# Performance work log

Measured on AMD Instinct MI355X. Metric: run time of the kernel, lower is better.

The kernel has to match this reference:

```python
import jax, jax.numpy as jnp
import numpy as np

N_NODES = 50000
N_EDGES = 1600000
NEG_SLOPE = 0.2


def setup_inputs() -> dict:
    key = jax.random.key(0)
    ks = jax.random.split(key, 11)
    s = 0.1  # small init scale
    return {
        "x": jax.random.normal(ks[0], (N_NODES, 128), dtype=jnp.float32),
        "edge_index": jax.random.randint(ks[1], (2, N_EDGES), 0, N_NODES, dtype=jnp.int64),
        "W1": jax.random.normal(ks[2], (128, 128), dtype=jnp.float32) * s,
        "att_src1": jax.random.normal(ks[3], (2, 64), dtype=jnp.float32) * s,
        "att_dst1": jax.random.normal(ks[4], (2, 64), dtype=jnp.float32) * s,
        "b1": jax.random.normal(ks[5], (128,), dtype=jnp.float32) * s,
        "W2": jax.random.normal(ks[6], (128, 64), dtype=jnp.float32) * s,
        "att_src2": jax.random.normal(ks[7], (1, 64), dtype=jnp.float32) * s,
        "att_dst2": jax.random.normal(ks[8], (1, 64), dtype=jnp.float32) * s,
        "b2": jax.random.normal(ks[9], (64,), dtype=jnp.float32) * s,
    }


def gat_conv(x, W, a_src, a_dst, bias, src, dst, n_nodes):
    # x: [N, F_in]; W: [F_in, H*C]; a_src/a_dst: [H, C]; bias: [H*C]
    H, C = a_src.shape
    xl = (x @ W).reshape(n_nodes, H, C)                 # [N,H,C]
    alpha_s = jnp.einsum('nhc,hc->nh', xl, a_src)       # [N,H]
    alpha_d = jnp.einsum('nhc,hc->nh', xl, a_dst)       # [N,H]
    e = jax.nn.leaky_relu(alpha_s[src] + alpha_d[dst], NEG_SLOPE)  # [E,H]
    # segment softmax over edges sharing the same destination node
    m = jax.ops.segment_max(e, dst, num_segments=n_nodes)          # [N,H]
    m = jnp.where(jnp.isfinite(m), m, 0.0)
    e = jnp.exp(e - m[dst])
    denom = jax.ops.segment_sum(e, dst, num_segments=n_nodes)      # [N,H]
    alpha = e / denom[dst]                               # self-loops guarantee denom > 0
    msg = xl[src] * alpha[:, :, None]                    # [E,H,C]
    out = jax.ops.segment_sum(msg, dst, num_segments=n_nodes)      # [N,H,C]
    return out.reshape(n_nodes, H * C) + bias


def reference(x, edge_index, W1, att_src1, att_dst1, b1, W2, att_src2, att_dst2, b2):
    n = x.shape[0]
    # PyG GATConv default add_self_loops=True
    loops = jnp.arange(n, dtype=edge_index.dtype)
    src = jnp.concatenate([edge_index[0], loops])
    dst = jnp.concatenate([edge_index[1], loops])

    h = gat_conv(x, W1, att_src1, att_dst1, b1, src, dst, n)   # [N, 128]
    h = jax.nn.relu(h)                                          # dropout p=0 (eval)
    h = gat_conv(h, W2, att_src2, att_dst2, b2, src, dst, n)   # [N, 64]
    h = jax.nn.relu(h)
    return h
```

## Files before the change

kernel.cpp:

```cpp
#include <hip/hip_runtime.h>
#include <cstdint>
#include <cstddef>

#define NEG_SLOPE 0.2f

#define NB 512
#define LOG_NB 9
#define MAXK 512

__device__ inline unsigned short f2bf(float f) {
    unsigned int u = __float_as_uint(f);
    u += 0x7FFFu + ((u >> 16) & 1u);
    return (unsigned short)(u >> 16);
}
__device__ inline float bf_lo(unsigned int u) { return __uint_as_float(u << 16); }
__device__ inline float bf_hi(unsigned int u) { return __uint_as_float(u & 0xFFFF0000u); }

__global__ __launch_bounds__(256) void sort_count_kernel(const int* __restrict__ ei, int E,
                                                         int K, int CH, int* __restrict__ bcnt) {
    __shared__ int hist[MAXK];
    int tid = threadIdx.x;
    for (int i = tid; i < K; i += 256) hist[i] = 0;
    __syncthreads();
    int lo = blockIdx.x * CH;
    int hi = lo + CH; if (hi > E) hi = E;
    for (int e = lo + tid; e < hi; e += 256)
        atomicAdd(&hist[ei[(size_t)E + e] >> LOG_NB], 1);
    __syncthreads();
    for (int i = tid; i < K; i += 256)
        if (hist[i]) atomicAdd(&bcnt[i], hist[i]);
}

__global__ void sort_scan_kernel(const int* __restrict__ bcnt, int* __restrict__ boff,
                                 int* __restrict__ bcur, int K, int E) {
    __shared__ int buf[MAXK];
    int tid = threadIdx.x;
    int v = (tid < K) ? bcnt[tid] : 0;
    buf[tid] = v;
    __syncthreads();
    for (int o = 1; o < MAXK; o <<= 1) {
        int t = (tid >= o) ? buf[tid - o] : 0;
        __syncthreads();
        buf[tid] += t;
        __syncthreads();
    }
    if (tid < K) {
        int ex = buf[tid] - v;
        boff[tid] = ex;
        bcur[tid] = ex;
    }
    if (tid == K) boff[K] = E;
}

__global__ __launch_bounds__(256) void sort_scatter_kernel(const int* __restrict__ ei, int E,
                                                           int K, int CH, int* __restrict__ bcur,
                                                           unsigned int* __restrict__ bkt) {
    __shared__ int hist[MAXK];
    __shared__ int base[MAXK];
    int tid = threadIdx.x;
    for (int i = tid; i < K; i += 256) hist[i] = 0;
    __syncthreads();
    int lo = blockIdx.x * CH;
    int hi = lo + CH; if (hi > E) hi = E;
    for (int e = lo + tid; e < hi; e += 256)
        atomicAdd(&hist[ei[(size_t)E + e] >> LOG_NB], 1);
    __syncthreads();
    for (int i = tid; i < K; i += 256) {
        int c = hist[i];
        base[i] = c ? atomicAdd(&bcur[i], c) : 0;
    }
    __syncthreads();
    for (int i = tid; i < K; i += 256) hist[i] = 0;
    __syncthreads();
    for (int e = lo + tid; e < hi; e += 256) {
        int s = ei[e];
        int d = ei[(size_t)E + e];
        int k = d >> LOG_NB;
        int r = atomicAdd(&hist[k], 1);
        bkt[(size_t)base[k] + r] = (unsigned int)s | ((unsigned int)d << 16);
    }
}

__global__ __launch_bounds__(256) void sort_finalize_kernel(const unsigned int* __restrict__ bkt,
                                                            const int* __restrict__ boff,
                                                            int* __restrict__ off,
                                                            int* __restrict__ csrc, int N) {
    __shared__ int nhist[NB];
    __shared__ int part[256];
    __shared__ int loff[NB];
    int k = blockIdx.x;
    int tid = threadIdx.x;
    int node0 = k << LOG_NB;
    int nh = N - node0; if (nh > NB) nh = NB;
    int beg = boff[k], end = boff[k + 1];
    for (int i = tid; i < NB; i += 256) nhist[i] = 0;
    __syncthreads();
    for (int e = beg + tid; e < end; e += 256)
        atomicAdd(&nhist[(bkt[e] >> 16) - node0], 1);
    __syncthreads();
    int i0 = 2 * tid, i1 = 2 * tid + 1;
    int v0 = (i0 < nh) ? nhist[i0] + 1 : 0;
    int v1 = (i1 < nh) ? nhist[i1] + 1 : 0;
    part[tid] = v0 + v1;
    __syncthreads();
    for (int o = 1; o < 256; o <<= 1) {
        int t = (tid >= o) ? part[tid - o] : 0;
        __syncthreads();
        part[tid] += t;
        __syncthreads();
    }
    int gbase = beg + node0;
    int base = gbase + ((tid > 0) ? part[tid - 1] : 0);
    if (i0 < nh) loff[i0] = base;
    if (i1 < nh) loff[i1] = base + v0;
    __syncthreads();
    for (int i = tid; i < nh; i += 256) {
        off[node0 + i] = loff[i];
        csrc[loff[i]] = node0 + i;
        nhist[i] = loff[i] + 1;
    }
    if (node0 + nh == N && tid == 0) off[N] = gbase + part[255];
    __syncthreads();
    for (int e = beg + tid; e < end; e += 256) {
        unsigned int p = bkt[e];
        int pos = atomicAdd(&nhist[(p >> 16) - node0], 1);
        csrc[pos] = (int)(p & 0xFFFFu);
    }
}


template <int FOUT, int H>
__global__ __launch_bounds__(256) void gemm_att_kernel(const float* __restrict__ X,
                                                       const float* __restrict__ W,
                                                       const float* __restrict__ attS,
                                                       const float* __restrict__ attD,
                                                       unsigned short* __restrict__ Ybf,
                                                       float* __restrict__ as_,
                                                       float* __restrict__ ad_, int N) {
    constexpr int ROWS = 8192 / FOUT;
    constexpr int CG   = FOUT / 4;
    __shared__ float sX[ROWS][68];
    __shared__ float sW[64 * FOUT];
    int tid = threadIdx.x;
    int rowbase = blockIdx.x * ROWS;
    int cg = tid % CG;
    int rg = tid / CG;
    int r0 = rg * 8;

    float acc[8][4];
#pragma unroll
    for (int i = 0; i < 8; i++)
#pragma unroll
        for (int c = 0; c < 4; c++) acc[i][c] = 0.f;

    for (int k0 = 0; k0 < 128; k0 += 64) {
        __syncthreads();
        for (int idx = tid; idx < ROWS * 16; idx += 256) {
            int r = idx >> 4, q = idx & 15;
            int row = rowbase + r;
            float4 val = (row < N) ? *(const float4*)&X[(size_t)row * 128 + k0 + q * 4]
                                   : make_float4(0.f, 0.f, 0.f, 0.f);
            *(float4*)&sX[r][q * 4] = val;
        }
        for (int idx = tid; idx < 16 * FOUT; idx += 256)
            *(float4*)&sW[idx * 4] = *(const float4*)&W[(size_t)k0 * FOUT + idx * 4];
        __syncthreads();
        for (int k = 0; k < 64; k += 4) {
            float4 xr[8];
#pragma unroll
            for (int i = 0; i < 8; i++)
                xr[i] = *(const float4*)&sX[r0 + i][k];
#pragma unroll
            for (int kk = 0; kk < 4; kk++) {
                float4 wv = ((const float4*)(sW + (size_t)(k + kk) * FOUT))[cg];
#pragma unroll
                for (int i = 0; i < 8; i++) {
                    float xv = (&xr[i].x)[kk];
                    acc[i][0] = fmaf(xv, wv.x, acc[i][0]);
                    acc[i][1] = fmaf(xv, wv.y, acc[i][1]);
                    acc[i][2] = fmaf(xv, wv.z, acc[i][2]);
                    acc[i][3] = fmaf(xv, wv.w, acc[i][3]);
                }
            }
        }
    }

#pragma unroll
    for (int i = 0; i < 8; i++) {
        int row = rowbase + r0 + i;
        if (row < N) {
            ushort4 v;
            v.x = f2bf(acc[i][0]); v.y = f2bf(acc[i][1]);
            v.z = f2bf(acc[i][2]); v.w = f2bf(acc[i][3]);
            *(ushort4*)(Ybf + (size_t)row * FOUT + cg * 4) = v;
        }
    }

    float4 asv = ((const float4*)attS)[cg];
    float4 adv = ((const float4*)attD)[cg];
    int head = (H == 2) ? (cg >> 4) : 0;
#pragma unroll
    for (int i = 0; i < 8; i++) {
        float ps = acc[i][0] * asv.x + acc[i][1] * asv.y + acc[i][2] * asv.z + acc[i][3] * asv.w;
        float pd = acc[i][0] * adv.x + acc[i][1] * adv.y + acc[i][2] * adv.z + acc[i][3] * adv.w;
#pragma unroll
        for (int o = 1; o <= 8; o <<= 1) { ps += __shfl_xor(ps, o); pd += __shfl_xor(pd, o); }
        int row = rowbase + r0 + i;
        if ((tid & 15) == 0 && row < N) {
            as_[(size_t)row * H + head] = ps;
            ad_[(size_t)row * H + head] = pd;
        }
    }
}


__global__ __launch_bounds__(256) void agg1_kernel(const unsigned short* __restrict__ xl,
                                                   const float* __restrict__ as_,
                                                   const float* __restrict__ ad_,
                                                   const float* __restrict__ bias,
                                                   const int* __restrict__ off,
                                                   const int* __restrict__ csrc,
                                                   float* __restrict__ out, int N) {
    __shared__ float4 sps[4][64];
    int wiw  = threadIdx.x >> 6;
    int lane = threadIdx.x & 63;
    int node = blockIdx.x * 4 + wiw;
    if (node >= N) return;
    int beg = off[node], end = off[node + 1];
    int deg = end - beg;
    float2 adn = ((const float2*)ad_)[node];

    int cl  = lane & 15;
    int sub = lane >> 4;
    int hd1 = (cl >> 3) & 1;
    float acc[8];
#pragma unroll
    for (int i = 0; i < 8; i++) acc[i] = 0.f;
    const uint4* xq = (const uint4*)xl + cl;

    if (deg <= 64) {
        int s = 0;
        float t0 = -1e30f, t1 = -1e30f;
        if (lane < deg) {
            s = csrc[beg + lane];
            float2 asv = ((const float2*)as_)[s];
            t0 = asv.x + adn.x; t0 = t0 > 0.f ? t0 : NEG_SLOPE * t0;
            t1 = asv.y + adn.y; t1 = t1 > 0.f ? t1 : NEG_SLOPE * t1;
        }
        float m0 = t0, m1 = t1;
#pragma unroll
        for (int o = 32; o; o >>= 1) {
            m0 = fmaxf(m0, __shfl_xor(m0, o));
            m1 = fmaxf(m1, __shfl_xor(m1, o));
        }
        float e0 = (lane < deg) ? __expf(t0 - m0) : 0.f;
        float e1 = (lane < deg) ? __expf(t1 - m1) : 0.f;
        float s0 = e0, s1 = e1;
#pragma unroll
        for (int o = 32; o; o >>= 1) { s0 += __shfl_xor(s0, o); s1 += __shfl_xor(s1, o); }
        sps[wiw][lane] = make_float4(e0 / s0, e1 / s1, __int_as_float(s), 0.f);
#pragma unroll
        for (int j = 0; j < 16; j++) {
            float4 q = sps[wiw][j * 4 + sub];
            float a  = hd1 ? q.y : q.x;
            int   sj = __float_as_int(q.z);
            uint4 v  = xq[(size_t)sj * 16];
            acc[0] = fmaf(a, bf_lo(v.x), acc[0]); acc[1] = fmaf(a, bf_hi(v.x), acc[1]);
            acc[2] = fmaf(a, bf_lo(v.y), acc[2]); acc[3] = fmaf(a, bf_hi(v.y), acc[3]);
            acc[4] = fmaf(a, bf_lo(v.z), acc[4]); acc[5] = fmaf(a, bf_hi(v.z), acc[5]);
            acc[6] = fmaf(a, bf_lo(v.w), acc[6]); acc[7] = fmaf(a, bf_hi(v.w), acc[7]);
        }
    } else {
        float m0 = -1e30f, m1 = -1e30f;
        for (int b = beg; b < end; b += 64) {
            int e = b + lane;
            if (e < end) {
                int s = csrc[e];
                float2 asv = ((const float2*)as_)[s];
                float t0 = asv.x + adn.x; t0 = t0 > 0.f ? t0 : NEG_SLOPE * t0;
                float t1 = asv.y + adn.y; t1 = t1 > 0.f ? t1 : NEG_SLOPE * t1;
                m0 = fmaxf(m0, t0); m1 = fmaxf(m1, t1);
            }
        }
#pragma unroll
        for (int o = 32; o; o >>= 1) {
            m0 = fmaxf(m0, __shfl_xor(m0, o));
            m1 = fmaxf(m1, __shfl_xor(m1, o));
        }
        float s0 = 0.f, s1 = 0.f;
        for (int b = beg; b < end; b += 64) {
            int e = b + lane;
            if (e < end) {
                int s = csrc[e];
                float2 asv = ((const float2*)as_)[s];
                float t0 = asv.x + adn.x; t0 = t0 > 0.f ? t0 : NEG_SLOPE * t0;
                float t1 = asv.y + adn.y; t1 = t1 > 0.f ? t1 : NEG_SLOPE * t1;
                s0 += __expf(t0 - m0); s1 += __expf(t1 - m1);
            }
        }
#pragma unroll
        for (int o = 32; o; o >>= 1) { s0 += __shfl_xor(s0, o); s1 += __shfl_xor(s1, o); }
        float i0 = 1.f / s0, i1 = 1.f / s1;
        for (int b = beg; b < end; b += 64) {
            int cnt = end - b; if (cnt > 64) cnt = 64;
            float p0 = 0.f, p1 = 0.f; int s = 0;
            if (lane < cnt) {
                s = csrc[b + lane];
                float2 asv = ((const float2*)as_)[s];
                float t0 = asv.x + adn.x; t0 = t0 > 0.f ? t0 : NEG_SLOPE * t0;
                float t1 = asv.y + adn.y; t1 = t1 > 0.f ? t1 : NEG_SLOPE * t1;
                p0 = __expf(t0 - m0) * i0; p1 = __expf(t1 - m1) * i1;
            }
            sps[wiw][lane] = make_float4(p0, p1, __int_as_float(s), 0.f);
#pragma unroll
            for (int j = 0; j < 16; j++) {
                float4 q = sps[wiw][j * 4 + sub];
                float a  = hd1 ? q.y : q.x;
                int   sj = __float_as_int(q.z);
                uint4 v  = xq[(size_t)sj * 16];
                acc[0] = fmaf(a, bf_lo(v.x), acc[0]); acc[1] = fmaf(a, bf_hi(v.x), acc[1]);
                acc[2] = fmaf(a, bf_lo(v.y), acc[2]); acc[3] = fmaf(a, bf_hi(v.y), acc[3]);
                acc[4] = fmaf(a, bf_lo(v.z), acc[4]); acc[5] = fmaf(a, bf_hi(v.z), acc[5]);
                acc[6] = fmaf(a, bf_lo(v.w), acc[6]); acc[7] = fmaf(a, bf_hi(v.w), acc[7]);
            }
        }
    }
#pragma unroll
    for (int o = 16; o <= 32; o <<= 1)
#pragma unroll
        for (int i = 0; i < 8; i++) acc[i] += __shfl_xor(acc[i], o);
    if (sub == 0) {
        float* op = out + (size_t)node * 128 + cl * 8;
        const float* bp = bias + cl * 8;
#pragma unroll
        for (int i = 0; i < 8; i++) op[i] = fmaxf(acc[i] + bp[i], 0.f);
    }
}


__global__ __launch_bounds__(256) void agg2_kernel(const unsigned short* __restrict__ xl,
                                                   const float* __restrict__ as_,
                                                   const float* __restrict__ ad_,
                                                   const float* __restrict__ bias,
                                                   const int* __restrict__ off,
                                                   const int* __restrict__ csrc,
                                                   float* __restrict__ out, int N) {
    __shared__ float2 sps[4][64];
    int wiw  = threadIdx.x >> 6;
    int lane = threadIdx.x & 63;
    int node = blockIdx.x * 4 + wiw;
    if (node >= N) return;
    int beg = off[node], end = off[node + 1];
    int deg = end - beg;
    float adn = ad_[node];

    int cl  = lane & 7;
    int sub = lane >> 3;
    float acc[8];
#pragma unroll
    for (int i = 0; i < 8; i++) acc[i] = 0.f;
    const uint4* xq = (const uint4*)xl + cl;

    if (deg <= 64) {
        int s = 0;
        float t = -1e30f;
        if (lane < deg) {
            s = csrc[beg + lane];
            t = as_[s] + adn;
            t = t > 0.f ? t : NEG_SLOPE * t;
        }
        float m = t;
#pragma unroll
        for (int o = 32; o; o >>= 1) m = fmaxf(m, __shfl_xor(m, o));
        float ev = (lane < deg) ? __expf(t - m) : 0.f;
        float sum = ev;
#pragma unroll
        for (int o = 32; o; o >>= 1) sum += __shfl_xor(sum, o);
        sps[wiw][lane] = make_float2(ev / sum, __int_as_float(s));
#pragma unroll
        for (int j = 0; j < 8; j++) {
            float2 q = sps[wiw][j * 8 + sub];
            float a  = q.x;
            int   sj = __float_as_int(q.y);
            uint4 v  = xq[(size_t)sj * 8];
            acc[0] = fmaf(a, bf_lo(v.x), acc[0]); acc[1] = fmaf(a, bf_hi(v.x), acc[1]);
            acc[2] = fmaf(a, bf_lo(v.y), acc[2]); acc[3] = fmaf(a, bf_hi(v.y), acc[3]);
            acc[4] = fmaf(a, bf_lo(v.z), acc[4]); acc[5] = fmaf(a, bf_hi(v.z), acc[5]);
            acc[6] = fmaf(a, bf_lo(v.w), acc[6]); acc[7] = fmaf(a, bf_hi(v.w), acc[7]);
        }
    } else {
        float m = -1e30f;
        for (int b = beg; b < end; b += 64) {
            int e = b + lane;
            if (e < end) {
                float t = as_[csrc[e]] + adn;
                t = t > 0.f ? t : NEG_SLOPE * t;
                m = fmaxf(m, t);
            }
        }
#pragma unroll
        for (int o = 32; o; o >>= 1) m = fmaxf(m, __shfl_xor(m, o));
        float sum = 0.f;
        for (int b = beg; b < end; b += 64) {
            int e = b + lane;
            if (e < end) {
                float t = as_[csrc[e]] + adn;
                t = t > 0.f ? t : NEG_SLOPE * t;
                sum += __expf(t - m);
            }
        }
#pragma unroll
        for (int o = 32; o; o >>= 1) sum += __shfl_xor(sum, o);
        float inv = 1.f / sum;
        for (int b = beg; b < end; b += 64) {
            int cnt = end - b; if (cnt > 64) cnt = 64;
            float p = 0.f; int s = 0;
            if (lane < cnt) {
                s = csrc[b + lane];
                float t = as_[s] + adn;
                t = t > 0.f ? t : NEG_SLOPE * t;
                p = __expf(t - m) * inv;
            }
            sps[wiw][lane] = make_float2(p, __int_as_float(s));
#pragma unroll
            for (int j = 0; j < 8; j++) {
                float2 q = sps[wiw][j * 8 + sub];
                float a  = q.x;
                int   sj = __float_as_int(q.y);
                uint4 v  = xq[(size_t)sj * 8];
                acc[0] = fmaf(a, bf_lo(v.x), acc[0]); acc[1] = fmaf(a, bf_hi(v.x), acc[1]);
                acc[2] = fmaf(a, bf_lo(v.y), acc[2]); acc[3] = fmaf(a, bf_hi(v.y), acc[3]);
                acc[4] = fmaf(a, bf_lo(v.z), acc[4]); acc[5] = fmaf(a, bf_hi(v.z), acc[5]);
                acc[6] = fmaf(a, bf_lo(v.w), acc[6]); acc[7] = fmaf(a, bf_hi(v.w), acc[7]);
            }
        }
    }
#pragma unroll
    for (int o = 8; o <= 32; o <<= 1)
#pragma unroll
        for (int i = 0; i < 8; i++) acc[i] += __shfl_xor(acc[i], o);
    if (sub == 0) {
        float* op = out + (size_t)node * 64 + cl * 8;
        const float* bp = bias + cl * 8;
#pragma unroll
        for (int i = 0; i < 8; i++) op[i] = fmaxf(acc[i] + bp[i], 0.f);
    }
}


extern "C" void kernel_launch(void* const* d_in, const int* in_sizes, int n_in,
                              void* d_out, int out_size, void* d_ws, size_t ws_size,
                              hipStream_t stream) {
    const float* x        = (const float*)d_in[0];
    const int*   ei       = (const int*)d_in[1];
    const float* W1       = (const float*)d_in[2];
    const float* attS1    = (const float*)d_in[3];
    const float* attD1    = (const float*)d_in[4];
    const float* b1       = (const float*)d_in[5];
    const float* W2       = (const float*)d_in[6];
    const float* attS2    = (const float*)d_in[7];
    const float* attD2    = (const float*)d_in[8];
    const float* b2       = (const float*)d_in[9];
    float* out            = (float*)d_out;

    int N  = in_sizes[0] / 128;
    int E  = in_sizes[1] / 2;
    int EE = E + N;
    int K  = (N + NB - 1) >> LOG_NB;

    char* w = (char*)d_ws;
    auto alloc = [&](size_t bytes) -> void* {
        void* p = (void*)w;
        w += (bytes + 255) & ~(size_t)255;
        return p;
    };
    int*   bcnt = (int*)alloc((size_t)(K + 1) * 4);
    int*   boff = (int*)alloc((size_t)(K + 1) * 4);
    int*   bcur = (int*)alloc((size_t)(K + 1) * 4);
    int*   off  = (int*)alloc((size_t)(N + 1) * 4);
    int*   csrc = (int*)alloc((size_t)EE * 4);
    unsigned short* xl1 = (unsigned short*)alloc((size_t)N * 128 * 2);
    float* sd1  = (float*)alloc((size_t)N * 2 * 4);
    float* dd1  = (float*)alloc((size_t)N * 2 * 4);
    float* h1   = (float*)alloc((size_t)N * 128 * 4);

    unsigned int* bkt = (unsigned int*)xl1;
    unsigned short* xl2 = xl1;
    float* sd2 = sd1;
    float* dd2 = dd1;

    hipMemsetAsync(bcnt, 0, (size_t)(K + 1) * 4, stream);

    int G  = 256;
    int CH = (E + G - 1) / G;
    sort_count_kernel<<<G, 256, 0, stream>>>(ei, E, K, CH, bcnt);
    sort_scan_kernel<<<1, MAXK, 0, stream>>>(bcnt, boff, bcur, K, E);
    sort_scatter_kernel<<<G, 256, 0, stream>>>(ei, E, K, CH, bcur, bkt);
    sort_finalize_kernel<<<K, 256, 0, stream>>>(bkt, boff, off, csrc, N);

    gemm_att_kernel<128, 2><<<(N + 63) / 64, 256, 0, stream>>>(x, W1, attS1, attD1, xl1, sd1, dd1, N);
    agg1_kernel<<<(N + 3) / 4, 256, 0, stream>>>(xl1, sd1, dd1, b1, off, csrc, h1, N);

    gemm_att_kernel<64, 1><<<(N + 127) / 128, 256, 0, stream>>>(h1, W2, attS2, attD2, xl2, sd2, dd2, N);
    agg2_kernel<<<(N + 3) / 4, 256, 0, stream>>>(xl2, sd2, dd2, b2, off, csrc, out, N);
}
```

Measured before the change: 330.3 us.

## Precompute per-edge attention logits, store hidden layer in bf16, trim aggregation loops

Packs src and dst into each CSR entry and adds separate eval kernels that compute leaky-relu attention logits per edge ahead of aggregation. The aggregation kernels then read contiguous logits instead of gathering as_[src] three times per edge. The layer-1 output is stored as bf16 and the second GEMM reads bf16 input, halving that intermediate traffic. Small-degree loops now iterate only over valid edges instead of a fixed 16 or 8. This costs two extra launches and extra edge-sized buffers, and rounding h1 to bf16 adds precision loss.

Result: slower. 356.8 us (+8.0%).

```diff
diff --git a/kernel.cpp b/kernel.cpp
--- a/kernel.cpp
+++ b/kernel.cpp
@@ -15,6 +15,9 @@
 }
 __device__ inline float bf_lo(unsigned int u) { return __uint_as_float(u << 16); }
 __device__ inline float bf_hi(unsigned int u) { return __uint_as_float(u & 0xFFFF0000u); }
+__device__ inline unsigned int pk2bf(float lo, float hi) {
+    return (unsigned int)f2bf(lo) | ((unsigned int)f2bf(hi) << 16);
+}
 
 __global__ __launch_bounds__(256) void sort_count_kernel(const int* __restrict__ ei, int E,
                                                          int K, int CH, int* __restrict__ bcnt) {
@@ -84,7 +87,7 @@
 __global__ __launch_bounds__(256) void sort_finalize_kernel(const unsigned int* __restrict__ bkt,
                                                             const int* __restrict__ boff,
                                                             int* __restrict__ off,
-                                                            int* __restrict__ csrc, int N) {
+                                                            unsigned int* __restrict__ csrc, int N) {
     __shared__ int nhist[NB];
     __shared__ int part[256];
     __shared__ int loff[NB];
@@ -115,8 +118,9 @@
     if (i1 < nh) loff[i1] = base + v0;
     __syncthreads();
     for (int i = tid; i < nh; i += 256) {
-        off[node0 + i] = loff[i];
-        csrc[loff[i]] = node0 + i;
+        int node = node0 + i;
+        off[node] = loff[i];
+        csrc[loff[i]] = (unsigned int)node | ((unsigned int)node << 16);
         nhist[i] = loff[i] + 1;
     }
     if (node0 + nh == N && tid == 0) off[N] = gbase + part[255];
@@ -124,13 +128,13 @@
     for (int e = beg + tid; e < end; e += 256) {
         unsigned int p = bkt[e];
         int pos = atomicAdd(&nhist[(p >> 16) - node0], 1);
-        csrc[pos] = (int)(p & 0xFFFFu);
-    }
-}
-
-
-template <int FOUT, int H>
-__global__ __launch_bounds__(256) void gemm_att_kernel(const float* __restrict__ X,
+        csrc[pos] = p;
+    }
+}
+
+
+template <int FOUT, int H, bool BF16IN>
+__global__ __launch_bounds__(256) void gemm_att_kernel(const void* __restrict__ Xv,
                                                        const float* __restrict__ W,
                                                        const float* __restrict__ attS,
                                                        const float* __restrict__ attD,
@@ -155,12 +159,28 @@
 
     for (int k0 = 0; k0 < 128; k0 += 64) {
         __syncthreads();
-        for (int idx = tid; idx < ROWS * 16; idx += 256) {
-            int r = idx >> 4, q = idx & 15;
-            int row = rowbase + r;
-            float4 val = (row < N) ? *(const float4*)&X[(size_t)row * 128 + k0 + q * 4]
-                                   : make_float4(0.f, 0.f, 0.f, 0.f);
-            *(float4*)&sX[r][q * 4] = val;
+        if (BF16IN) {
+            const unsigned short* Xb = (const unsigned short*)Xv;
+            for (int idx = tid; idx < ROWS * 8; idx += 256) {
+                int r = idx >> 3, g = idx & 7;
+                int row = rowbase + r;
+                uint4 v = (row < N) ? *(const uint4*)&Xb[(size_t)row * 128 + k0 + g * 8]
+                                    : make_uint4(0, 0, 0, 0);
+                float* dst = &sX[r][g * 8];
+                dst[0] = bf_lo(v.x); dst[1] = bf_hi(v.x);
+                dst[2] = bf_lo(v.y); dst[3] = bf_hi(v.y);
+                dst[4] = bf_lo(v.z); dst[5] = bf_hi(v.z);
+                dst[6] = bf_lo(v.w); dst[7] = bf_hi(v.w);
+            }
+        } else {
+            const float* X = (const float*)Xv;
+            for (int idx = tid; idx < ROWS * 16; idx += 256) {
+                int r = idx >> 4, q = idx & 15;
+                int row = rowbase + r;
+                float4 val = (row < N) ? *(const float4*)&X[(size_t)row * 128 + k0 + q * 4]
+                                       : make_float4(0.f, 0.f, 0.f, 0.f);
+                *(float4*)&sX[r][q * 4] = val;
+            }
         }
         for (int idx = tid; idx < 16 * FOUT; idx += 256)
             *(float4*)&sW[idx * 4] = *(const float4*)&W[(size_t)k0 * FOUT + idx * 4];
@@ -214,13 +234,39 @@
 }
 
 
+__global__ __launch_bounds__(256) void eval1_kernel(const unsigned int* __restrict__ csrc,
+                                                    const float* __restrict__ as_,
+                                                    const float* __restrict__ ad_,
+                                                    float2* __restrict__ ev, int EE) {
+    int e = blockIdx.x * 256 + threadIdx.x;
+    if (e >= EE) return;
+    unsigned int u = csrc[e];
+    int s = u & 0xFFFFu, d = u >> 16;
+    float2 a = ((const float2*)as_)[s];
+    float2 b = ((const float2*)ad_)[d];
+    float t0 = a.x + b.x; t0 = t0 > 0.f ? t0 : NEG_SLOPE * t0;
+    float t1 = a.y + b.y; t1 = t1 > 0.f ? t1 : NEG_SLOPE * t1;
+    ev[e] = make_float2(t0, t1);
+}
+
+__global__ __launch_bounds__(256) void eval2_kernel(const unsigned int* __restrict__ csrc,
+                                                    const float* __restrict__ as_,
+                                                    const float* __restrict__ ad_,
+                                                    float* __restrict__ ev, int EE) {
+    int e = blockIdx.x * 256 + threadIdx.x;
+    if (e >= EE) return;
+    unsigned int u = csrc[e];
+    float t = as_[u & 0xFFFFu] + ad_[u >> 16];
+    ev[e] = t > 0.f ? t : NEG_SLOPE * t;
+}
+
+
 __global__ __launch_bounds__(256) void agg1_kernel(const unsigned short* __restrict__ xl,
-                                                   const float* __restrict__ as_,
-                                                   const float* __restrict__ ad_,
+                                                   const float2* __restrict__ ev,
                                                    const float* __restrict__ bias,
                                                    const int* __restrict__ off,
-                                                   const int* __restrict__ csrc,
-                                                   float* __restrict__ out, int N) {
+                                                   const unsigned int* __restrict__ csrc,
+                                                   unsigned short* __restrict__ out, int N) {
     __shared__ float4 sps[4][64];
     int wiw  = threadIdx.x >> 6;
     int lane = threadIdx.x & 63;
@@ -228,7 +274,6 @@
     if (node >= N) return;
     int beg = off[node], end = off[node + 1];
     int deg = end - beg;
-    float2 adn = ((const float2*)ad_)[node];
 
     int cl  = lane & 15;
     int sub = lane >> 4;
@@ -242,10 +287,9 @@
         int s = 0;
         float t0 = -1e30f, t1 = -1e30f;
         if (lane < deg) {
-            s = csrc[beg + lane];
-            float2 asv = ((const float2*)as_)[s];
-            t0 = asv.x + adn.x; t0 = t0 > 0.f ? t0 : NEG_SLOPE * t0;
-            t1 = asv.y + adn.y; t1 = t1 > 0.f ? t1 : NEG_SLOPE * t1;
+            s = (int)(csrc[beg + lane] & 0xFFFFu);
+            float2 t = ev[beg + lane];
+            t0 = t.x; t1 = t.y;
         }
         float m0 = t0, m1 = t1;
 #pragma unroll
@@ -259,8 +303,9 @@
 #pragma unroll
         for (int o = 32; o; o >>= 1) { s0 += __shfl_xor(s0, o); s1 += __shfl_xor(s1, o); }
         sps[wiw][lane] = make_float4(e0 / s0, e1 / s1, __int_as_float(s), 0.f);
-#pragma unroll
-        for (int j = 0; j < 16; j++) {
+        int iters = (deg + 3) >> 2;
+#pragma unroll 8
+        for (int j = 0; j < iters; j++) {
             float4 q = sps[wiw][j * 4 + sub];
             float a  = hd1 ? q.y : q.x;
             int   sj = __float_as_int(q.z);
@@ -275,11 +320,8 @@
         for (int b = beg; b < end; b += 64) {
             int e = b + lane;
             if (e < end) {
-                int s = csrc[e];
-                float2 asv = ((const float2*)as_)[s];
-                float t0 = asv.x + adn.x; t0 = t0 > 0.f ? t0 : NEG_SLOPE * t0;
-                float t1 = asv.y + adn.y; t1 = t1 > 0.f ? t1 : NEG_SLOPE * t1;
-                m0 = fmaxf(m0, t0); m1 = fmaxf(m1, t1);
+                float2 t = ev[e];
+                m0 = fmaxf(m0, t.x); m1 = fmaxf(m1, t.y);
             }
         }
 #pragma unroll
@@ -291,11 +333,8 @@
         for (int b = beg; b < end; b += 64) {
             int e = b + lane;
             if (e < end) {
-                int s = csrc[e];
-                float2 asv = ((const float2*)as_)[s];
-                float t0 = asv.x + adn.x; t0 = t0 > 0.f ? t0 : NEG_SLOPE * t0;
-                float t1 = asv.y + adn.y; t1 = t1 > 0.f ? t1 : NEG_SLOPE * t1;
-                s0 += __expf(t0 - m0); s1 += __expf(t1 - m1);
+                float2 t = ev[e];
+                s0 += __expf(t.x - m0); s1 += __expf(t.y - m1);
             }
         }
 #pragma unroll
@@ -305,15 +344,14 @@
             int cnt = end - b; if (cnt > 64) cnt = 64;
             float p0 = 0.f, p1 = 0.f; int s = 0;
             if (lane < cnt) {
-                s = csrc[b + lane];
-                float2 asv = ((const float2*)as_)[s];
-                float t0 = asv.x + adn.x; t0 = t0 > 0.f ? t0 : NEG_SLOPE * t0;
-                float t1 = asv.y + adn.y; t1 = t1 > 0.f ? t1 : NEG_SLOPE * t1;
-                p0 = __expf(t0 - m0) * i0; p1 = __expf(t1 - m1) * i1;
+                s = (int)(csrc[b + lane] & 0xFFFFu);
+                float2 t = ev[b + lane];
+                p0 = __expf(t.x - m0) * i0; p1 = __expf(t.y - m1) * i1;
             }
             sps[wiw][lane] = make_float4(p0, p1, __int_as_float(s), 0.f);
-#pragma unroll
-            for (int j = 0; j < 16; j++) {
+            int iters = (cnt + 3) >> 2;
+#pragma unroll 8
+            for (int j = 0; j < iters; j++) {
                 float4 q = sps[wiw][j * 4 + sub];
                 float a  = hd1 ? q.y : q.x;
                 int   sj = __float_as_int(q.z);
@@ -330,20 +368,23 @@
 #pragma unroll
         for (int i = 0; i < 8; i++) acc[i] += __shfl_xor(acc[i], o);
     if (sub == 0) {
-        float* op = out + (size_t)node * 128 + cl * 8;
         const float* bp = bias + cl * 8;
-#pragma unroll
-        for (int i = 0; i < 8; i++) op[i] = fmaxf(acc[i] + bp[i], 0.f);
+        uint4 pk;
+        float v0, v1;
+        v0 = fmaxf(acc[0] + bp[0], 0.f); v1 = fmaxf(acc[1] + bp[1], 0.f); pk.x = pk2bf(v0, v1);
+        v0 = fmaxf(acc[2] + bp[2], 0.f); v1 = fmaxf(acc[3] + bp[3], 0.f); pk.y = pk2bf(v0, v1);
+        v0 = fmaxf(acc[4] + bp[4], 0.f); v1 = fmaxf(acc[5] + bp[5], 0.f); pk.z = pk2bf(v0, v1);
+        v0 = fmaxf(acc[6] + bp[6], 0.f); v1 = fmaxf(acc[7] + bp[7], 0.f); pk.w = pk2bf(v0, v1);
+        *(uint4*)(out + (size_t)node * 128 + cl * 8) = pk;
     }
 }
 
 
 __global__ __launch_bounds__(256) void agg2_kernel(const unsigned short* __restrict__ xl,
-                                                   const float* __restrict__ as_,
-                                                   const float* __restrict__ ad_,
+                                                   const float* __restrict__ ev,
                                                    const float* __restrict__ bias,
                                                    const int* __restrict__ off,
-                                                   const int* __restrict__ csrc,
+                                                   const unsigned int* __restrict__ csrc,
                                                    float* __restrict__ out, int N) {
     __shared__ float2 sps[4][64];
     int wiw  = threadIdx.x >> 6;
@@ -352,7 +393,6 @@
     if (node >= N) return;
     int beg = off[node], end = off[node + 1];
     int deg = end - beg;
-    float adn = ad_[node];
 
     int cl  = lane & 7;
     int sub = lane >> 3;
@@ -365,20 +405,20 @@
         int s = 0;
         float t = -1e30f;
         if (lane < deg) {
-            s = csrc[beg + lane];
-            t = as_[s] + adn;
-            t = t > 0.f ? t : NEG_SLOPE * t;
+            s = (int)(csrc[beg + lane] & 0xFFFFu);
+            t = ev[beg + lane];
         }
         float m = t;
 #pragma unroll
         for (int o = 32; o; o >>= 1) m = fmaxf(m, __shfl_xor(m, o));
-        float ev = (lane < deg) ? __expf(t - m) : 0.f;
-        float sum = ev;
+        float evv = (lane < deg) ? __expf(t - m) : 0.f;
+        float sum = evv;
 #pragma unroll
         for (int o = 32; o; o >>= 1) sum += __shfl_xor(sum, o);
-        sps[wiw][lane] = make_float2(ev / sum, __int_as_float(s));
-#pragma unroll
-        for (int j = 0; j < 8; j++) {
+        sps[wiw][lane] = make_float2(evv / sum, __int_as_float(s));
+        int iters = (deg + 7) >> 3;
+#pragma unroll 8
+        for (int j = 0; j < iters; j++) {
             float2 q = sps[wiw][j * 8 + sub];
             float a  = q.x;
             int   sj = __float_as_int(q.y);
@@ -392,22 +432,14 @@
         float m = -1e30f;
         for (int b = beg; b < end; b += 64) {
             int e = b + lane;
-            if (e < end) {
-                float t = as_[csrc[e]] + adn;
-                t = t > 0.f ? t : NEG_SLOPE * t;
-                m = fmaxf(m, t);
-            }
+            if (e < end) m = fmaxf(m, ev[e]);
         }
 #pragma unroll
         for (int o = 32; o; o >>= 1) m = fmaxf(m, __shfl_xor(m, o));
         float sum = 0.f;
         for (int b = beg; b < end; b += 64) {
             int e = b + lane;
-            if (e < end) {
-                float t = as_[csrc[e]] + adn;
-                t = t > 0.f ? t : NEG_SLOPE * t;
-                sum += __expf(t - m);
-            }
+            if (e < end) sum += __expf(ev[e] - m);
         }
 #pragma unroll
         for (int o = 32; o; o >>= 1) sum += __shfl_xor(sum, o);
@@ -416,14 +448,13 @@
             int cnt = end - b; if (cnt > 64) cnt = 64;
             float p = 0.f; int s = 0;
             if (lane < cnt) {
-                s = csrc[b + lane];
-                float t = as_[s] + adn;
-                t = t > 0.f ? t : NEG_SLOPE * t;
-                p = __expf(t - m) * inv;
+                s = (int)(csrc[b + lane] & 0xFFFFu);
+                p = __expf(ev[b + lane] - m) * inv;
             }
             sps[wiw][lane] = make_float2(p, __int_as_float(s));
-#pragma unroll
-            for (int j = 0; j < 8; j++) {
+            int iters = (cnt + 7) >> 3;
+#pragma unroll 8
+            for (int j = 0; j < iters; j++) {
                 float2 q = sps[wiw][j * 8 + sub];
                 float a  = q.x;
                 int   sj = __float_as_int(q.y);
@@ -478,29 +509,34 @@
     int*   boff = (int*)alloc((size_t)(K + 1) * 4);
     int*   bcur = (int*)alloc((size_t)(K + 1) * 4);
     int*   off  = (int*)alloc((size_t)(N + 1) * 4);
-    int*   csrc = (int*)alloc((size_t)EE * 4);
+    unsigned int* csrc = (unsigned int*)alloc((size_t)EE * 4);
     unsigned short* xl1 = (unsigned short*)alloc((size_t)N * 128 * 2);
     float* sd1  = (float*)alloc((size_t)N * 2 * 4);
     float* dd1  = (float*)alloc((size_t)N * 2 * 4);
-    float* h1   = (float*)alloc((size_t)N * 128 * 4);
+    unsigned short* h1 = (unsigned short*)alloc((size_t)N * 128 * 2);
+    float2* ev1 = (float2*)alloc((size_t)EE * 8);
 
     unsigned int* bkt = (unsigned int*)xl1;
     unsigned short* xl2 = xl1;
     float* sd2 = sd1;
     float* dd2 = dd1;
+    float* ev2 = (float*)ev1;
 
     hipMemsetAsync(bcnt, 0, (size_t)(K + 1) * 4, stream);
 
     int G  = 256;
     int CH = (E + G - 1) / G;
+    int GE = (EE + 255) / 256;
     sort_count_kernel<<<G, 256, 0, stream>>>(ei, E, K, CH, bcnt);
     sort_scan_kernel<<<1, MAXK, 0, stream>>>(bcnt, boff, bcur, K, E);
     sort_scatter_kernel<<<G, 256, 0, stream>>>(ei, E, K, CH, bcur, bkt);
     sort_finalize_kernel<<<K, 256, 0, stream>>>(bkt, boff, off, csrc, N);
 
-    gemm_att_kernel<128, 2><<<(N + 63) / 64, 256, 0, stream>>>(x, W1, attS1, attD1, xl1, sd1, dd1, N);
-    agg1_kernel<<<(N + 3) / 4, 256, 0, stream>>>(xl1, sd1, dd1, b1, off, csrc, h1, N);
-
-    gemm_att_kernel<64, 1><<<(N + 127) / 128, 256, 0, stream>>>(h1, W2, attS2, attD2, xl2, sd2, dd2, N);
-    agg2_kernel<<<(N + 3) / 4, 256, 0, stream>>>(xl2, sd2, dd2, b2, off, csrc, out, N);
-}
+    gemm_att_kernel<128, 2, false><<<(N + 63) / 64, 256, 0, stream>>>(x, W1, attS1, attD1, xl1, sd1, dd1, N);
+    eval1_kernel<<<GE, 256, 0, stream>>>(csrc, sd1, dd1, ev1, EE);
+    agg1_kernel<<<(N + 3) / 4, 256, 0, stream>>>(xl1, ev1, b1, off, csrc, h1, N);
+
+    gemm_att_kernel<64, 1, true><<<(N + 127) / 128, 256, 0, stream>>>(h1, W2, attS2, attD2, xl2, sd2, dd2, N);
+    eval2_kernel<<<GE, 256, 0, stream>>>(csrc, sd2, dd2, ev2, EE);
+    agg2_kernel<<<(N + 3) / 4, 256, 0, stream>>>(xl2, ev2, b2, off, csrc, out, N);
+}
```
